# Kernel optimization log

Measured on AMD Instinct MI355X. Metric: run time of the kernel, lower is better.

## Reference

```python
import jax, jax.numpy as jnp
import numpy as np

B, N, D = 8, 4096, 1024
DEPTH, HEADS, DH = 4, 16, 64
INNER = HEADS * DH          # 1024
NL, NMP = 64, 4             # latents, mean-pooled latents
FF = 4 * D                  # ff_mult=4
EPS = 1e-5


def _ln(x, w, b):
    # nn.LayerNorm over last dim (eps added to biased variance)
    m = x.mean(-1, keepdims=True)
    v = ((x - m) ** 2).mean(-1, keepdims=True)
    return (x - m) * jax.lax.rsqrt(v + EPS) * w + b


def _ln_g(x, g):
    # custom LayerNorm: gamma only, no bias
    m = x.mean(-1, keepdims=True)
    v = ((x - m) ** 2).mean(-1, keepdims=True)
    return (x - m) * jax.lax.rsqrt(v + EPS) * g


def setup_inputs() -> dict:
    key = jax.random.key(0)
    ks = jax.random.split(key, 16)
    g = lambda i, shape: jax.random.normal(ks[i], shape, jnp.float32) * 0.02
    return dict(
        x=jax.random.normal(ks[0], (B, N, D), jnp.float32),
        pos_emb=g(1, (N, D)),                      # rows [0:N] of the embedding table
        latents=jax.random.normal(ks[2], (NL, D), jnp.float32),
        mp_ln_g=jnp.ones((D,), jnp.float32),
        mp_w=g(3, (D, D * NMP)),
        mp_b=jnp.zeros((D * NMP,), jnp.float32),
        ln_x_w=jnp.ones((DEPTH, D), jnp.float32),
        ln_x_b=jnp.zeros((DEPTH, D), jnp.float32),
        ln_lat_w=jnp.ones((DEPTH, D), jnp.float32),
        ln_lat_b=jnp.zeros((DEPTH, D), jnp.float32),
        wq=g(4, (DEPTH, D, INNER)),
        wkv=g(5, (DEPTH, D, 2 * INNER)),
        wo=g(6, (DEPTH, INNER, D)),
        out_ln_w=jnp.ones((DEPTH, D), jnp.float32),
        out_ln_b=jnp.zeros((DEPTH, D), jnp.float32),
        ff_ln1_g=jnp.ones((DEPTH, D), jnp.float32),
        ff_w1=g(7, (DEPTH, D, FF)),
        ff_ln2_g=jnp.ones((DEPTH, FF), jnp.float32),
        ff_w2=g(8, (DEPTH, FF, D)),
    )


def reference(x, pos_emb, latents, mp_ln_g, mp_w, mp_b,
              ln_x_w, ln_x_b, ln_lat_w, ln_lat_b, wq, wkv, wo,
              out_ln_w, out_ln_b, ff_ln1_g, ff_w1, ff_ln2_g, ff_w2):
    b = x.shape[0]
    xp = x + pos_emb                                  # (b, n, d)
    lat = jnp.broadcast_to(latents, (b,) + latents.shape)
    # mean-pooled latents (mask is all-ones -> plain mean over tokens)
    mp = x.mean(axis=1)                               # (b, d)
    mp_lat = (_ln_g(mp, mp_ln_g) @ mp_w + mp_b).reshape(b, NMP, D)
    lat = jnp.concatenate([mp_lat, lat], axis=1)      # (b, NMP+NL, d)
    scale = DH ** -0.5
    for l in range(DEPTH):
        # --- PerceiverAttention ---
        xn = _ln(xp, ln_x_w[l], ln_x_b[l])
        ln_lat = _ln(lat, ln_lat_w[l], ln_lat_b[l])
        q = (ln_lat @ wq[l]).reshape(b, -1, HEADS, DH) * scale   # (b, i, h, dh)
        kv = jnp.concatenate([xn, ln_lat], axis=1) @ wkv[l]      # (b, n+i, 2*inner)
        k, v = jnp.split(kv, 2, axis=-1)
        k = k.reshape(b, -1, HEADS, DH)
        v = v.reshape(b, -1, HEADS, DH)
        sim = jnp.einsum('bihd,bjhd->bhij', q, k)                # (b, h, i, n+i)
        attn = jax.nn.softmax(sim, axis=-1)
        o = jnp.einsum('bhij,bjhd->bihd', attn, v).reshape(b, -1, INNER)
        o = _ln(o @ wo[l], out_ln_w[l], out_ln_b[l])
        lat = lat + o
        # --- feedforward block ---
        h = jax.nn.gelu(_ln_g(lat, ff_ln1_g[l]) @ ff_w1[l], approximate=False)
        lat = lat + _ln_g(h, ff_ln2_g[l]) @ ff_w2[l]
    return lat
```

## Files before the change

kernel.cpp:

```cpp
#include <hip/hip_runtime.h>

typedef __bf16 bf16x8 __attribute__((ext_vector_type(8)));
typedef float f32x4 __attribute__((ext_vector_type(4)));
typedef unsigned short u16;
typedef unsigned int u32;

typedef __attribute__((address_space(3))) u16 lds_u16;
typedef __attribute__((address_space(1))) const u16 glb_u16;

#define NJC 4

__device__ inline float bf2f(u16 u) { union { u32 i; float f; } x; x.i = (u32)u << 16; return x.f; }
__device__ inline u16 f2bf(float f) {
  union { float f; u32 i; } u; u.f = f;
  u32 r = u.i + 0x7fffu + ((u.i >> 16) & 1u);
  return (u16)(r >> 16);
}

__device__ inline float blk_sum256(float v, float* red) {
#pragma unroll
  for (int o = 32; o > 0; o >>= 1) v += __shfl_xor(v, o);
  __syncthreads();
  if ((threadIdx.x & 63) == 0) red[threadIdx.x >> 6] = v;
  __syncthreads();
  return red[0] + red[1] + red[2] + red[3];
}

__global__ __launch_bounds__(512, 1) void gemm_kv(const u16* __restrict__ A,
                                                  const u16* __restrict__ BT,
                                                  u16* __restrict__ C,
                                                  const float* __restrict__ bias) {
  extern __shared__ __align__(16) u16 lds[];
  const int tid = threadIdx.x, l = tid & 63, w = tid >> 6;
  const int wr = w >> 2, wc = w & 3;
  int bid = blockIdx.x;
  int swz = (bid & 7) * 128 + (bid >> 3);
  int by = swz >> 3, bx = swz & 7;
  const long m0 = (long)by * 256;
  const int n0 = bx * 256;

  long srcA[2], srcB[2];
#pragma unroll
  for (int s = 0; s < 2; s++) {
    int g = s * 512 + tid;
    int p = g >> 3, j = g & 7, jp = j ^ (p & 7);
    int row = (p << 1) | (jp >> 2), cc = jp & 3;
    srcA[s] = (m0 + row) * 1024 + cc * 8;
    srcB[s] = ((long)(n0 + row)) * 1024 + cc * 8;
  }
  const int ldsoff[2] = { (w * 64) * 8, (512 + w * 64) * 8 };

  const int rA = l & 15, cch = l >> 4;
  const int R0a = wr * 128 + rA;
  const int aoff = (R0a >> 1) * 64 + (((((R0a & 1) << 2) | cch) ^ ((R0a >> 1) & 7)) << 3);
  const int R0b = wc * 64 + rA;
  const int boff = (R0b >> 1) * 64 + (((((R0b & 1) << 2) | cch) ^ ((R0b >> 1) & 7)) << 3);

  f32x4 acc[8][4] = {};

  auto stage = [&](int t, int ab) {
    u16* dst = lds + (((t & 3) * 2 + ab) << 13);
    const u16* src = ab == 0 ? A : BT;
    const long* so = ab == 0 ? srcA : srcB;
    int kt = t * 32;
#pragma unroll
    for (int s = 0; s < 2; s++)
      __builtin_amdgcn_global_load_lds((glb_u16*)(src + so[s] + kt),
                                       (lds_u16*)(dst + ldsoff[s]), 16, 0, 0);
  };

  stage(0, 0); stage(0, 1); stage(1, 0); stage(1, 1); stage(2, 0); stage(2, 1);
  asm volatile("s_waitcnt vmcnt(8)" ::: "memory");
  __builtin_amdgcn_s_barrier();

  for (int t = 0; t < 16; ++t) {
    const int s = 2 * t;
    const u16* Ab0 = lds + (((s & 3) * 2 + 0) << 13);
    const u16* Bb0 = lds + (((s & 3) * 2 + 1) << 13);
    const u16* Ab1 = lds + ((((s + 1) & 3) * 2 + 0) << 13);
    const u16* Bb1 = lds + ((((s + 1) & 3) * 2 + 1) << 13);
    bf16x8 af[8], b0, b1;

#pragma unroll
    for (int mf = 0; mf < 8; mf++) af[mf] = *(const bf16x8*)(Ab0 + aoff + mf * 512);
    b0 = *(const bf16x8*)(Bb0 + boff);
    b1 = *(const bf16x8*)(Bb0 + boff + 512);
    if (s + 3 < 32) stage(s + 3, 0);
    __builtin_amdgcn_s_barrier();
    asm volatile("s_waitcnt lgkmcnt(0)" ::: "memory");
    __builtin_amdgcn_sched_barrier(0);
    __builtin_amdgcn_s_setprio(1);
#pragma unroll
    for (int mf = 0; mf < 8; mf++) {
      acc[mf][0] = __builtin_amdgcn_mfma_f32_16x16x32_bf16(af[mf], b0, acc[mf][0], 0, 0, 0);
      acc[mf][1] = __builtin_amdgcn_mfma_f32_16x16x32_bf16(af[mf], b1, acc[mf][1], 0, 0, 0);
    }
    __builtin_amdgcn_s_setprio(0);
    __builtin_amdgcn_s_barrier();

    b0 = *(const bf16x8*)(Bb0 + boff + 1024);
    b1 = *(const bf16x8*)(Bb0 + boff + 1536);
    if (s + 3 < 32) stage(s + 3, 1);
    __builtin_amdgcn_s_barrier();
    asm volatile("s_waitcnt lgkmcnt(0)" ::: "memory");
    __builtin_amdgcn_sched_barrier(0);
    __builtin_amdgcn_s_setprio(1);
#pragma unroll
    for (int mf = 0; mf < 8; mf++) {
      acc[mf][2] = __builtin_amdgcn_mfma_f32_16x16x32_bf16(af[mf], b0, acc[mf][2], 0, 0, 0);
      acc[mf][3] = __builtin_amdgcn_mfma_f32_16x16x32_bf16(af[mf], b1, acc[mf][3], 0, 0, 0);
    }
    __builtin_amdgcn_s_setprio(0);
    if (t < 15) asm volatile("s_waitcnt vmcnt(8)" ::: "memory");
    else        asm volatile("s_waitcnt vmcnt(0)" ::: "memory");
    __builtin_amdgcn_s_barrier();

#pragma unroll
    for (int mf = 0; mf < 8; mf++) af[mf] = *(const bf16x8*)(Ab1 + aoff + mf * 512);
    b0 = *(const bf16x8*)(Bb1 + boff);
    b1 = *(const bf16x8*)(Bb1 + boff + 512);
    if (s + 4 < 32) stage(s + 4, 0);
    __builtin_amdgcn_s_barrier();
    asm volatile("s_waitcnt lgkmcnt(0)" ::: "memory");
    __builtin_amdgcn_sched_barrier(0);
    __builtin_amdgcn_s_setprio(1);
#pragma unroll
    for (int mf = 0; mf < 8; mf++) {
      acc[mf][0] = __builtin_amdgcn_mfma_f32_16x16x32_bf16(af[mf], b0, acc[mf][0], 0, 0, 0);
      acc[mf][1] = __builtin_amdgcn_mfma_f32_16x16x32_bf16(af[mf], b1, acc[mf][1], 0, 0, 0);
    }
    __builtin_amdgcn_s_setprio(0);
    __builtin_amdgcn_s_barrier();

    b0 = *(const bf16x8*)(Bb1 + boff + 1024);
    b1 = *(const bf16x8*)(Bb1 + boff + 1536);
    if (s + 4 < 32) stage(s + 4, 1);
    __builtin_amdgcn_s_barrier();
    asm volatile("s_waitcnt lgkmcnt(0)" ::: "memory");
    __builtin_amdgcn_sched_barrier(0);
    __builtin_amdgcn_s_setprio(1);
#pragma unroll
    for (int mf = 0; mf < 8; mf++) {
      acc[mf][2] = __builtin_amdgcn_mfma_f32_16x16x32_bf16(af[mf], b0, acc[mf][2], 0, 0, 0);
      acc[mf][3] = __builtin_amdgcn_mfma_f32_16x16x32_bf16(af[mf], b1, acc[mf][3], 0, 0, 0);
    }
    __builtin_amdgcn_s_setprio(0);
    if (t < 14)       asm volatile("s_waitcnt vmcnt(8)" ::: "memory");
    else if (t == 14) asm volatile("s_waitcnt vmcnt(4)" ::: "memory");
    __builtin_amdgcn_s_barrier();
  }

  const long batch_off = (m0 >> 12) * ((long)4164 * 2048);
  const int rb0 = (int)(m0 & 4095) + wr * 128 + ((l >> 4) << 2);
#pragma unroll
  for (int mf = 0; mf < 8; mf++) {
#pragma unroll
    for (int nf = 0; nf < 4; nf++) {
      int col = n0 + wc * 64 + nf * 16 + (l & 15);
      float bv = bias[col];
#pragma unroll
      for (int rr = 0; rr < 4; rr++) {
        int rloc = rb0 + mf * 16 + rr;
        C[batch_off + (long)rloc * 2048 + col] = f2bf(acc[mf][nf][rr] + bv);
      }
    }
  }
}

template <int MODE, bool BIAS>
__global__ __launch_bounds__(256) void gemm_nt(const u16* __restrict__ A,
                                               const u16* __restrict__ BT,
                                               void* __restrict__ C,
                                               const float* __restrict__ bias,
                                               int M, int N, int K, float alpha,
                                               int RB, long BS, int LDC, int KC) {
  __shared__ __align__(16) u16 As[2][128 * 64];
  __shared__ __align__(16) u16 Bs[2][128 * 64];
  int m0 = blockIdx.y * 128, n0 = blockIdx.x * 128;
  int tid = threadIdx.x;
  int l = tid & 63, w = tid >> 6;
  int wr = w >> 1, wc = w & 1;
  f32x4 acc[4][4] = {};

  const int srow = l >> 3;
  const int scol = (l & 7) * 8;
  const int Mc = M - 1;
  const int k0 = blockIdx.z * KC;
  const int k1 = (k0 + KC < K) ? k0 + KC : K;

  auto stage = [&](int kt, int pb) {
#pragma unroll
    for (int r = 0; r < 4; r++) {
      int rowg = (r * 4 + w) * 8;
      int arow = m0 + rowg + srow; if (arow > Mc) arow = Mc;
      int brow = n0 + rowg + srow;
      const u16* ag = A + (long)arow * K + kt + scol;
      const u16* bg = BT + (long)brow * K + kt + scol;
      __builtin_amdgcn_global_load_lds((glb_u16*)ag, (lds_u16*)(&As[pb][rowg * 64]), 16, 0, 0);
      __builtin_amdgcn_global_load_lds((glb_u16*)bg, (lds_u16*)(&Bs[pb][rowg * 64]), 16, 0, 0);
    }
  };

  stage(k0, 0);
  int it = 0;
  for (int kt = k0; kt < k1; kt += 64, ++it) {
    const int pb = it & 1;
    const bool more = (kt + 64) < k1;
    if (more) stage(kt + 64, pb ^ 1);
    if (more) asm volatile("s_waitcnt vmcnt(8)" ::: "memory");
    else      asm volatile("s_waitcnt vmcnt(0)" ::: "memory");
    __builtin_amdgcn_sched_barrier(0);
    __builtin_amdgcn_s_barrier();
    const u16* Ab = &As[pb][0];
    const u16* Bb = &Bs[pb][0];
#pragma unroll
    for (int kk = 0; kk < 2; kk++) {
      bf16x8 af[4], bfv[4];
#pragma unroll
      for (int mf = 0; mf < 4; mf++)
        af[mf] = *(const bf16x8*)(Ab + (wr * 64 + mf * 16 + (l & 15)) * 64 + kk * 32 + (l >> 4) * 8);
#pragma unroll
      for (int nf = 0; nf < 4; nf++)
        bfv[nf] = *(const bf16x8*)(Bb + (wc * 64 + nf * 16 + (l & 15)) * 64 + kk * 32 + (l >> 4) * 8);
#pragma unroll
      for (int mf = 0; mf < 4; mf++)
#pragma unroll
        for (int nf = 0; nf < 4; nf++)
          acc[mf][nf] = __builtin_amdgcn_mfma_f32_16x16x32_bf16(af[mf], bfv[nf], acc[mf][nf], 0, 0, 0);
    }
    __builtin_amdgcn_sched_barrier(0);
    __builtin_amdgcn_s_barrier();
  }

#pragma unroll
  for (int mf = 0; mf < 4; mf++) {
#pragma unroll
    for (int nf = 0; nf < 4; nf++) {
      int col = n0 + wc * 64 + nf * 16 + (l & 15);
      float bv = 0.f;
      if (BIAS) bv = bias[col];
#pragma unroll
      for (int rr = 0; rr < 4; rr++) {
        int row = m0 + wr * 64 + mf * 16 + (l >> 4) * 4 + rr;
        if (row < M) {
          float v = acc[mf][nf][rr] * alpha + bv;
          long off = (long)(row / RB) * BS + (long)(row % RB) * LDC + col;
          if (MODE == 0) ((float*)C)[off] = v;
          else if (MODE == 1) ((u16*)C)[off] = f2bf(v);
          else if (MODE == 2) ((float*)C)[off] += v;
          else atomicAdd(&((float*)C)[off], v);
        }
      }
    }
  }
}

__global__ __launch_bounds__(256) void gemm_two(const u16* __restrict__ A,
                                                const u16* __restrict__ BTq,
                                                const u16* __restrict__ BTkv,
                                                u16* __restrict__ Cq,
                                                u16* __restrict__ Ckv) {
  __shared__ __align__(16) u16 As[2][128 * 64];
  __shared__ __align__(16) u16 Bs[2][128 * 64];
  const int K = 1024, M = 544;
  int bxr = blockIdx.x;
  const u16* BT; u16* C; float alpha; int RB; long BS; int LDC; int n0;
  if (bxr < 8) { BT = BTq;  C = Cq;  alpha = 0.125f; RB = 544; BS = 0;                 LDC = 1024; n0 = bxr * 128; }
  else         { BT = BTkv; C = Ckv; alpha = 1.f;    RB = 68;  BS = (long)4164 * 2048; LDC = 2048; n0 = (bxr - 8) * 128; }
  int m0 = blockIdx.y * 128;
  int tid = threadIdx.x;
  int l = tid & 63, w = tid >> 6;
  int wr = w >> 1, wc = w & 1;
  f32x4 acc[4][4] = {};

  const int srow = l >> 3;
  const int scol = (l & 7) * 8;
  const int Mc = M - 1;

  auto stage = [&](int kt, int pb) {
#pragma unroll
    for (int r = 0; r < 4; r++) {
      int rowg = (r * 4 + w) * 8;
      int arow = m0 + rowg + srow; if (arow > Mc) arow = Mc;
      int brow = n0 + rowg + srow;
      const u16* ag = A + (long)arow * K + kt + scol;
      const u16* bg = BT + (long)brow * K + kt + scol;
      __builtin_amdgcn_global_load_lds((glb_u16*)ag, (lds_u16*)(&As[pb][rowg * 64]), 16, 0, 0);
      __builtin_amdgcn_global_load_lds((glb_u16*)bg, (lds_u16*)(&Bs[pb][rowg * 64]), 16, 0, 0);
    }
  };

  stage(0, 0);
  int it = 0;
  for (int kt = 0; kt < K; kt += 64, ++it) {
    const int pb = it & 1;
    const bool more = (kt + 64) < K;
    if (more) stage(kt + 64, pb ^ 1);
    if (more) asm volatile("s_waitcnt vmcnt(8)" ::: "memory");
    else      asm volatile("s_waitcnt vmcnt(0)" ::: "memory");
    __builtin_amdgcn_sched_barrier(0);
    __builtin_amdgcn_s_barrier();
    const u16* Ab = &As[pb][0];
    const u16* Bb = &Bs[pb][0];
#pragma unroll
    for (int kk = 0; kk < 2; kk++) {
      bf16x8 af[4], bfv[4];
#pragma unroll
      for (int mf = 0; mf < 4; mf++)
        af[mf] = *(const bf16x8*)(Ab + (wr * 64 + mf * 16 + (l & 15)) * 64 + kk * 32 + (l >> 4) * 8);
#pragma unroll
      for (int nf = 0; nf < 4; nf++)
        bfv[nf] = *(const bf16x8*)(Bb + (wc * 64 + nf * 16 + (l & 15)) * 64 + kk * 32 + (l >> 4) * 8);
#pragma unroll
      for (int mf = 0; mf < 4; mf++)
#pragma unroll
        for (int nf = 0; nf < 4; nf++)
          acc[mf][nf] = __builtin_amdgcn_mfma_f32_16x16x32_bf16(af[mf], bfv[nf], acc[mf][nf], 0, 0, 0);
    }
    __builtin_amdgcn_sched_barrier(0);
    __builtin_amdgcn_s_barrier();
  }

#pragma unroll
  for (int mf = 0; mf < 4; mf++) {
#pragma unroll
    for (int nf = 0; nf < 4; nf++) {
      int col = n0 + wc * 64 + nf * 16 + (l & 15);
#pragma unroll
      for (int rr = 0; rr < 4; rr++) {
        int row = m0 + wr * 64 + mf * 16 + (l >> 4) * 4 + rr;
        if (row < M) {
          float v = acc[mf][nf][rr] * alpha;
          long off = (long)(row / RB) * BS + (long)(row % RB) * LDC + col;
          C[off] = f2bf(v);
        }
      }
    }
  }
}

__global__ __launch_bounds__(256) void k_transpose(const float* __restrict__ W,
                                                   const float* __restrict__ scale,
                                                   u16* __restrict__ WT, int K, int N,
                                                   long wls, long sls, long tls) {
  __shared__ float tile[32][33];
  int z = blockIdx.z;
  W += (long)z * wls; WT += (long)z * tls;
  if (scale) scale += (long)z * sls;
  int n0 = blockIdx.x * 32, k0 = blockIdx.y * 32;
  int x = threadIdx.x, y = threadIdx.y;
#pragma unroll
  for (int i = 0; i < 4; i++) tile[y + 8 * i][x] = W[(long)(k0 + y + 8 * i) * N + n0 + x];
  __syncthreads();
#pragma unroll
  for (int i = 0; i < 4; i++) {
    int k = k0 + x, n = n0 + y + 8 * i;
    float v = tile[x][y + 8 * i];
    if (scale) v *= scale[k];
    WT[(long)n * K + k] = f2bf(v);
  }
}

__global__ __launch_bounds__(256) void k_transpose2(const float* __restrict__ W,
                                                    const float* __restrict__ scale,
                                                    u16* __restrict__ WTs,
                                                    u16* __restrict__ WTp, int K, int N,
                                                    long wls, long sls, long tls) {
  __shared__ float tile[32][33];
  int z = blockIdx.z;
  W += (long)z * wls; scale += (long)z * sls;
  WTs += (long)z * tls; WTp += (long)z * tls;
  int n0 = blockIdx.x * 32, k0 = blockIdx.y * 32;
  int x = threadIdx.x, y = threadIdx.y;
#pragma unroll
  for (int i = 0; i < 4; i++) tile[y + 8 * i][x] = W[(long)(k0 + y + 8 * i) * N + n0 + x];
  __syncthreads();
#pragma unroll
  for (int i = 0; i < 4; i++) {
    int k = k0 + x, n = n0 + y + 8 * i;
    float v = tile[x][y + 8 * i];
    WTp[(long)n * K + k] = f2bf(v);
    WTs[(long)n * K + k] = f2bf(v * scale[k]);
  }
}

__global__ __launch_bounds__(256) void k_xphat(const float* __restrict__ x,
                                               const float* __restrict__ pos,
                                               u16* __restrict__ xph) {
  __shared__ float red[4];
  long row = blockIdx.x;
  int n = blockIdx.x & 4095;
  const float* xr = x + row * 1024;
  const float* pr = pos + (long)n * 1024;
  float v[4]; float s = 0.f;
#pragma unroll
  for (int i = 0; i < 4; i++) { int c = threadIdx.x + i * 256; v[i] = xr[c] + pr[c]; s += v[i]; }
  float mean = blk_sum256(s, red) * (1.f / 1024.f);
  float s2 = 0.f;
#pragma unroll
  for (int i = 0; i < 4; i++) { float d = v[i] - mean; s2 += d * d; }
  float rs = rsqrtf(blk_sum256(s2, red) * (1.f / 1024.f) + 1e-5f);
#pragma unroll
  for (int i = 0; i < 4; i++) xph[row * 1024 + threadIdx.x + i * 256] = f2bf((v[i] - mean) * rs);
}

__global__ __launch_bounds__(256) void k_mp(const float* __restrict__ x, float* __restrict__ macc) {
  int d = blockIdx.x * 256 + threadIdx.x;
  int nc = blockIdx.y, b = blockIdx.z;
  const float* xb = x + (long)b * 4096 * 1024;
  float s = 0.f;
  for (int n = nc * 256; n < nc * 256 + 256; n++) s += xb[(long)n * 1024 + d];
  atomicAdd(&macc[b * 1024 + d], s);
}

__global__ __launch_bounds__(256) void k_mphat(const float* __restrict__ macc,
                                               const float* __restrict__ g,
                                               float* __restrict__ mphat) {
  __shared__ float red[4];
  int b = blockIdx.x;
  float v[4]; float s = 0.f;
#pragma unroll
  for (int i = 0; i < 4; i++) { v[i] = macc[b * 1024 + threadIdx.x + i * 256] * (1.f / 4096.f); s += v[i]; }
  float mean = blk_sum256(s, red) * (1.f / 1024.f);
  float s2 = 0.f;
#pragma unroll
  for (int i = 0; i < 4; i++) { float d = v[i] - mean; s2 += d * d; }
  float rs = rsqrtf(blk_sum256(s2, red) * (1.f / 1024.f) + 1e-5f);
#pragma unroll
  for (int i = 0; i < 4; i++) {
    int c = threadIdx.x + i * 256;
    mphat[b * 1024 + c] = (v[i] - mean) * rs * g[c];
  }
}

__global__ __launch_bounds__(256) void k_mplat(const float* __restrict__ mphat,
                                               const float* __restrict__ w,
                                               const float* __restrict__ bias,
                                               float* __restrict__ lat) {
  int j = blockIdx.x * 256 + threadIdx.x;
  int b = blockIdx.y;
  const float* mh = mphat + b * 1024;
  float s = bias[j];
  for (int k = 0; k < 1024; k++) s += mh[k] * w[(long)k * 4096 + j];
  lat[(long)b * 69632 + (j >> 10) * 1024 + (j & 1023)] = s;
}

__global__ __launch_bounds__(256) void k_latfill(const float* __restrict__ latents,
                                                 float* __restrict__ lat) {
  int idx = blockIdx.x * 256 + threadIdx.x;
  int b = idx >> 16, rest = idx & 65535;
  lat[(long)b * 69632 + 4096 + rest] = latents[rest];
}

__global__ __launch_bounds__(256) void k_lnrow(const float* __restrict__ in,
                                               const float* __restrict__ w,
                                               const float* __restrict__ bb,
                                               u16* __restrict__ out) {
  __shared__ float red[4];
  long row = blockIdx.x;
  const float* xr = in + row * 1024;
  float v[4]; float s = 0.f;
#pragma unroll
  for (int i = 0; i < 4; i++) { v[i] = xr[threadIdx.x + i * 256]; s += v[i]; }
  float mean = blk_sum256(s, red) * (1.f / 1024.f);
  float s2 = 0.f;
#pragma unroll
  for (int i = 0; i < 4; i++) { float d = v[i] - mean; s2 += d * d; }
  float rs = rsqrtf(blk_sum256(s2, red) * (1.f / 1024.f) + 1e-5f);
#pragma unroll
  for (int i = 0; i < 4; i++) {
    int c = threadIdx.x + i * 256;
    out[row * 1024 + c] = f2bf((v[i] - mean) * rs * w[c] + bb[c]);
  }
}

__global__ __launch_bounds__(256) void k_bias1(const float* __restrict__ wkv,
                                               const float* __restrict__ lnxb,
                                               float* __restrict__ bxp,
                                               long wls, long bls, long pls) {
  int z = blockIdx.z;
  wkv += (long)z * wls; lnxb += (long)z * bls; bxp += (long)z * pls;
  int n = blockIdx.x * 256 + threadIdx.x;
  int kc = blockIdx.y;
  float s = 0.f;
  for (int k = kc * 64; k < kc * 64 + 64; k++) s += lnxb[k] * wkv[(long)k * 2048 + n];
  bxp[kc * 2048 + n] = s;
}
__global__ __launch_bounds__(256) void k_bias2(const float* __restrict__ bxp,
                                               float* __restrict__ bx,
                                               long pls, long xls) {
  int z = blockIdx.y;
  bxp += (long)z * pls; bx += (long)z * xls;
  int n = blockIdx.x * 256 + threadIdx.x;
  float s = 0.f;
#pragma unroll
  for (int kc = 0; kc < 16; kc++) s += bxp[kc * 2048 + n];
  bx[n] = s;
}

__global__ __launch_bounds__(256) void k_flash(const u16* __restrict__ q,
                                               const u16* __restrict__ kv,
                                               float* __restrict__ opart,
                                               float* __restrict__ lpart) {
  int c = blockIdx.x, h = blockIdx.y, b = blockIdx.z;
  int tid = threadIdx.x, l = tid & 63, w = tid >> 6;

  __shared__ __align__(16) char smem_raw[46080];
  u16 (*Vt)[64][40] = reinterpret_cast<u16(*)[64][40]>(smem_raw);
  u16 (*Pl)[80][40] = reinterpret_cast<u16(*)[80][40]>(smem_raw + 20480);
  float (*O_s)[64] = reinterpret_cast<float(*)[64]>(smem_raw);
  float* l_s = reinterpret_cast<float*>(smem_raw + 20480);

  const int JCH = 1041;
  const int jstart = c * JCH;
  const int jend = (c == NJC - 1) ? 4164 : jstart + JCH;
  const long kvbase = (long)b * 4164 * 2048;
  const u16* Kp = kv + kvbase + h * 64;
  const u16* Vp = kv + kvbase + 1024 + h * 64;

  bf16x8 qf[5][2];
#pragma unroll
  for (int it = 0; it < 5; it++) {
    int qi = it * 16 + (l & 15); if (qi > 67) qi = 67;
    const u16* qrow = q + ((long)(b * 68 + qi) * 1024 + h * 64 + (l >> 4) * 8);
    qf[it][0] = *(const bf16x8*)(qrow);
    qf[it][1] = *(const bf16x8*)(qrow + 32);
  }

  f32x4 Of[5][4] = {};
  float lac[5] = {0.f, 0.f, 0.f, 0.f, 0.f};

  auto loadV = [&](int j0, uint4 vv[4]) {
#pragma unroll
    for (int t = 0; t < 4; t++) {
      int vj = j0 + (l & 31);
      int vjc = vj < 4163 ? vj : 4163;
      int vd = (l >> 5) * 8 + t * 16;
      vv[t] = *(const uint4*)(Vp + (long)vjc * 2048 + vd);
    }
  };
  auto loadK = [&](int j0, bf16x8& a00, bf16x8& a01, bf16x8& a10, bf16x8& a11) {
    const u16* kr0 = Kp + (long)(j0 + (l & 15)) * 2048 + (l >> 4) * 8;
    a00 = *(const bf16x8*)(kr0);
    a01 = *(const bf16x8*)(kr0 + 32);
    const u16* kr1 = Kp + (long)(j0 + 16 + (l & 15)) * 2048 + (l >> 4) * 8;
    a10 = *(const bf16x8*)(kr1);
    a11 = *(const bf16x8*)(kr1 + 32);
  };

  const int jbeg = jstart + w * 32;
  uint4 vr[4];
  bf16x8 k0a, k0b, k1a, k1b;
  if (jbeg < jend) { loadV(jbeg, vr); loadK(jbeg, k0a, k0b, k1a, k1b); }

  for (int j0 = jbeg; j0 < jend; j0 += 4 * 32) {
#pragma unroll
    for (int t = 0; t < 4; t++) {
      int vd = (l >> 5) * 8 + t * 16;
      union { uint4 q4; u16 s[8]; } uu; uu.q4 = vr[t];
#pragma unroll
      for (int e = 0; e < 8; e++) Vt[w][vd + e][l & 31] = uu.s[e];
    }
    f32x4 sf[2][5];
#pragma unroll
    for (int it = 0; it < 5; it++) {
      f32x4 d0 = {};
      d0 = __builtin_amdgcn_mfma_f32_16x16x32_bf16(k0a, qf[it][0], d0, 0, 0, 0);
      d0 = __builtin_amdgcn_mfma_f32_16x16x32_bf16(k0b, qf[it][1], d0, 0, 0, 0);
      sf[0][it] = d0;
      f32x4 d1 = {};
      d1 = __builtin_amdgcn_mfma_f32_16x16x32_bf16(k1a, qf[it][0], d1, 0, 0, 0);
      d1 = __builtin_amdgcn_mfma_f32_16x16x32_bf16(k1b, qf[it][1], d1, 0, 0, 0);
      sf[1][it] = d1;
    }
    int jn = j0 + 4 * 32;
    bool more = jn < jend;
    uint4 vr2[4];
    bf16x8 n0a, n0b, n1a, n1b;
    if (more) { loadV(jn, vr2); loadK(jn, n0a, n0b, n1a, n1b); }
#pragma unroll
    for (int jt = 0; jt < 2; jt++) {
      int jb = j0 + jt * 16 + (l >> 4) * 4;
#pragma unroll
      for (int it = 0; it < 5; it++) {
        u16 pk[4];
#pragma unroll
        for (int r = 0; r < 4; r++) {
          float p = (jb + r < jend) ? __expf(sf[jt][it][r]) : 0.f;
          lac[it] += p;
          pk[r] = f2bf(p);
        }
        *(uint2*)(&Pl[w][it * 16 + (l & 15)][jt * 16 + (l >> 4) * 4]) = *(const uint2*)pk;
      }
    }
#pragma unroll
    for (int it = 0; it < 5; it++) {
      bf16x8 pa = *(const bf16x8*)(&Pl[w][it * 16 + (l & 15)][(l >> 4) * 8]);
#pragma unroll
      for (int dt = 0; dt < 4; dt++) {
        bf16x8 vb = *(const bf16x8*)(&Vt[w][dt * 16 + (l & 15)][(l >> 4) * 8]);
        Of[it][dt] = __builtin_amdgcn_mfma_f32_16x16x32_bf16(pa, vb, Of[it][dt], 0, 0, 0);
      }
    }
    if (more) {
      vr[0] = vr2[0]; vr[1] = vr2[1]; vr[2] = vr2[2]; vr[3] = vr2[3];
      k0a = n0a; k0b = n0b; k1a = n1a; k1b = n1b;
    }
  }

  __syncthreads();
  for (int u = tid; u < 80 * 64; u += 256) ((float*)O_s)[u] = 0.f;
  if (tid < 80) l_s[tid] = 0.f;
  __syncthreads();
#pragma unroll
  for (int it = 0; it < 5; it++) {
    float v = lac[it];
    v += __shfl_xor(v, 16);
    v += __shfl_xor(v, 32);
    if (l < 16) atomicAdd(&l_s[it * 16 + l], v);
#pragma unroll
    for (int dt = 0; dt < 4; dt++) {
#pragma unroll
      for (int r = 0; r < 4; r++) {
        int i = it * 16 + (l >> 4) * 4 + r;
        int d = dt * 16 + (l & 15);
        atomicAdd(&O_s[i][d], Of[it][dt][r]);
      }
    }
  }
  __syncthreads();
  long base = (long)((b * 16 + h) * NJC + c);
  for (int u = tid; u < 68 * 64; u += 256)
    opart[base * 68 * 64 + u] = O_s[u >> 6][u & 63];
  if (tid < 68) lpart[base * 68 + tid] = l_s[tid];
}

__global__ __launch_bounds__(256) void k_comb(const float* __restrict__ opart,
                                              const float* __restrict__ lpart,
                                              u16* __restrict__ obf,
                                              float* __restrict__ o2z) {
  int r = blockIdx.x;
  int b = r / 68, i = r % 68;
#pragma unroll
  for (int it = 0; it < 4; it++) {
    int col = threadIdx.x + it * 256;
    int h = col >> 6, d = col & 63;
    long bh = (long)(b * 16 + h) * NJC;
    float os = 0.f, ls = 0.f;
    for (int cc = 0; cc < NJC; cc++) {
      os += opart[(bh + cc) * 68 * 64 + (long)i * 64 + d];
      ls += lpart[(bh + cc) * 68 + i];
    }
    obf[(long)r * 1024 + col] = f2bf(os / ls);
    o2z[(long)r * 1024 + col] = 0.f;
  }
}

__global__ __launch_bounds__(256) void k_attnln(const float* __restrict__ o2,
                                                float* __restrict__ lat,
                                                const float* __restrict__ w,
                                                const float* __restrict__ bb,
                                                const float* __restrict__ g,
                                                u16* __restrict__ latg) {
  __shared__ float red[4];
  long row = blockIdx.x;
  const float* xr = o2 + row * 1024;
  float* lr = lat + row * 1024;
  float v[4]; float s = 0.f;
#pragma unroll
  for (int i = 0; i < 4; i++) { v[i] = xr[threadIdx.x + i * 256]; s += v[i]; }
  float mean = blk_sum256(s, red) * (1.f / 1024.f);
  float s2 = 0.f;
#pragma unroll
  for (int i = 0; i < 4; i++) { float d = v[i] - mean; s2 += d * d; }
  float rs = rsqrtf(blk_sum256(s2, red) * (1.f / 1024.f) + 1e-5f);
  float lv[4]; float sl = 0.f;
#pragma unroll
  for (int i = 0; i < 4; i++) {
    int c = threadIdx.x + i * 256;
    float t = (v[i] - mean) * rs * w[c] + bb[c];
    lv[i] = lr[c] + t;
    lr[c] = lv[i];
    sl += lv[i];
  }
  float mean2 = blk_sum256(sl, red) * (1.f / 1024.f);
  float s22 = 0.f;
#pragma unroll
  for (int i = 0; i < 4; i++) { float d = lv[i] - mean2; s22 += d * d; }
  float rs2 = rsqrtf(blk_sum256(s22, red) * (1.f / 1024.f) + 1e-5f);
#pragma unroll
  for (int i = 0; i < 4; i++) {
    int c = threadIdx.x + i * 256;
    latg[row * 1024 + c] = f2bf((lv[i] - mean2) * rs2 * g[c]);
  }
}

__global__ __launch_bounds__(256) void k_geluln(const float* __restrict__ hin,
                                                const float* __restrict__ g,
                                                u16* __restrict__ out) {
  __shared__ float red[4];
  long row = blockIdx.x;
  const float* xr = hin + row * 4096;
  float v[16]; float s = 0.f;
#pragma unroll
  for (int i = 0; i < 16; i++) {
    int c = threadIdx.x + i * 256;
    float u = xr[c];
    u = 0.5f * u * (1.f + erff(u * 0.70710678118f));
    v[i] = u; s += u;
  }
  float mean = blk_sum256(s, red) * (1.f / 4096.f);
  float s2 = 0.f;
#pragma unroll
  for (int i = 0; i < 16; i++) { float d = v[i] - mean; s2 += d * d; }
  float rs = rsqrtf(blk_sum256(s2, red) * (1.f / 4096.f) + 1e-5f);
#pragma unroll
  for (int i = 0; i < 16; i++) {
    int c = threadIdx.x + i * 256;
    out[row * 4096 + c] = f2bf((v[i] - mean) * rs * g[c]);
  }
}

extern "C" void kernel_launch(void* const* d_in, const int* in_sizes, int n_in,
                              void* d_out, int out_size, void* d_ws, size_t ws_size,
                              hipStream_t stream) {
  const float* x    = (const float*)d_in[0];
  const float* pos  = (const float*)d_in[1];
  const float* lats = (const float*)d_in[2];
  const float* mplng= (const float*)d_in[3];
  const float* mpw  = (const float*)d_in[4];
  const float* mpb  = (const float*)d_in[5];
  const float* lnxw = (const float*)d_in[6];
  const float* lnxb = (const float*)d_in[7];
  const float* lnlw = (const float*)d_in[8];
  const float* lnlb = (const float*)d_in[9];
  const float* wq   = (const float*)d_in[10];
  const float* wkv  = (const float*)d_in[11];
  const float* wo   = (const float*)d_in[12];
  const float* olnw = (const float*)d_in[13];
  const float* olnb = (const float*)d_in[14];
  const float* ffg1 = (const float*)d_in[15];
  const float* ffw1 = (const float*)d_in[16];
  const float* ffg2 = (const float*)d_in[17];
  const float* ffw2 = (const float*)d_in[18];

  char* ws = (char*)d_ws;
  size_t off = 0;
  auto take = [&](size_t n) -> char* {
    off = (off + 255) & ~(size_t)255;
    char* p = ws + off; off += n; return p;
  };
  float* mp_acc = (float*)take(8 * 1024 * 4);
  float* mp_hat = (float*)take(8 * 1024 * 4);
  u16*   xp_hat = (u16*)take((size_t)8 * 4096 * 1024 * 2);
  float* lat    = (float*)take((size_t)8 * 68 * 1024 * 4);
  u16*   lnlat  = (u16*)take((size_t)544 * 1024 * 2);
  u16*   qb     = (u16*)take((size_t)544 * 1024 * 2);
  u16*   kvb    = (u16*)take(((size_t)8 * 4164 + 64) * 2048 * 2);
  float* opart  = (float*)take((size_t)128 * NJC * 68 * 64 * 4);
  float* lpart  = (float*)take((size_t)128 * NJC * 68 * 4);
  u16*   obf    = (u16*)take((size_t)544 * 1024 * 2);
  float* o2     = (float*)take((size_t)544 * 1024 * 4);
  u16*   latg   = (u16*)take((size_t)544 * 1024 * 2);
  float* hbuf   = (float*)take((size_t)544 * 4096 * 4);
  u16*   hg     = (u16*)take((size_t)544 * 4096 * 2);

  size_t fixed_off = off;
  u16 *wqT, *wkvxT, *wkvlT, *woT, *ffw1T, *ffw2T;
  float *bx, *bxp;
  auto alloc_w = [&](size_t rep) {
    wqT   = (u16*)take(rep * (size_t)1024 * 1024 * 2);
    wkvxT = (u16*)take(rep * (size_t)2048 * 1024 * 2);
    wkvlT = (u16*)take(rep * (size_t)2048 * 1024 * 2);
    woT   = (u16*)take(rep * (size_t)1024 * 1024 * 2);
    ffw1T = (u16*)take(rep * (size_t)4096 * 1024 * 2);
    ffw2T = (u16*)take(rep * (size_t)4096 * 1024 * 2);
    bx    = (float*)take(rep * 2048 * 4);
    bxp   = (float*)take(rep * 16 * 2048 * 4);
  };
  alloc_w(4);
  bool hoist = off <= ws_size;
  if (!hoist) { off = fixed_off; alloc_w(1); }

  const long KV_BS = (long)4164 * 2048;

  hipMemsetAsync(mp_acc, 0, 8 * 1024 * 4, stream);
  k_xphat<<<32768, 256, 0, stream>>>(x, pos, xp_hat);
  k_mp<<<dim3(4, 16, 8), 256, 0, stream>>>(x, mp_acc);
  k_mphat<<<8, 256, 0, stream>>>(mp_acc, mplng, mp_hat);
  k_mplat<<<dim3(16, 8), 256, 0, stream>>>(mp_hat, mpw, mpb, lat);
  k_latfill<<<2048, 256, 0, stream>>>(lats, lat);

  if (hoist) {
    k_transpose<<<dim3(32, 32, 4), dim3(32, 8), 0, stream>>>(
        wq, nullptr, wqT, 1024, 1024, 1048576, 0, 1048576);
    k_transpose2<<<dim3(64, 32, 4), dim3(32, 8), 0, stream>>>(
        wkv, lnxw, wkvxT, wkvlT, 1024, 2048, 2097152, 1024, 2097152);
    k_transpose<<<dim3(32, 32, 4), dim3(32, 8), 0, stream>>>(
        wo, nullptr, woT, 1024, 1024, 1048576, 0, 1048576);
    k_transpose<<<dim3(128, 32, 4), dim3(32, 8), 0, stream>>>(
        ffw1, nullptr, ffw1T, 1024, 4096, 4194304, 0, 4194304);
    k_transpose<<<dim3(32, 128, 4), dim3(32, 8), 0, stream>>>(
        ffw2, nullptr, ffw2T, 4096, 1024, 4194304, 0, 4194304);
    k_bias1<<<dim3(8, 16, 4), 256, 0, stream>>>(wkv, lnxb, bxp, 2097152, 1024, 32768);
    k_bias2<<<dim3(8, 4), 256, 0, stream>>>(bxp, bx, 32768, 2048);
  }

  for (int l = 0; l < 4; l++) {
    const float* wq_l  = wq  + (size_t)l * 1024 * 1024;
    const float* wkv_l = wkv + (size_t)l * 1024 * 2048;
    const float* wo_l  = wo  + (size_t)l * 1024 * 1024;
    const float* w1_l  = ffw1 + (size_t)l * 1024 * 4096;
    const float* w2_l  = ffw2 + (size_t)l * 4096 * 1024;

    if (!hoist) {
      k_transpose<<<dim3(32, 32, 1), dim3(32, 8), 0, stream>>>(
          wq_l, nullptr, wqT, 1024, 1024, 0, 0, 0);
      k_transpose2<<<dim3(64, 32, 1), dim3(32, 8), 0, stream>>>(
          wkv_l, lnxw + l * 1024, wkvxT, wkvlT, 1024, 2048, 0, 0, 0);
      k_transpose<<<dim3(32, 32, 1), dim3(32, 8), 0, stream>>>(
          wo_l, nullptr, woT, 1024, 1024, 0, 0, 0);
      k_transpose<<<dim3(128, 32, 1), dim3(32, 8), 0, stream>>>(
          w1_l, nullptr, ffw1T, 1024, 4096, 0, 0, 0);
      k_transpose<<<dim3(32, 128, 1), dim3(32, 8), 0, stream>>>(
          w2_l, nullptr, ffw2T, 4096, 1024, 0, 0, 0);
      k_bias1<<<dim3(8, 16, 1), 256, 0, stream>>>(wkv_l, lnxb + l * 1024, bxp, 0, 0, 0);
      k_bias2<<<dim3(8, 1), 256, 0, stream>>>(bxp, bx, 0, 0);
    }
    const u16* wqT_l   = wqT   + (hoist ? (size_t)l * 1048576 : 0);
    const u16* wkvxT_l = wkvxT + (hoist ? (size_t)l * 2097152 : 0);
    const u16* wkvlT_l = wkvlT + (hoist ? (size_t)l * 2097152 : 0);
    const u16* woT_l   = woT   + (hoist ? (size_t)l * 1048576 : 0);
    const u16* ffw1T_l = ffw1T + (hoist ? (size_t)l * 4194304 : 0);
    const u16* ffw2T_l = ffw2T + (hoist ? (size_t)l * 4194304 : 0);
    const float* bx_l  = bx    + (hoist ? (size_t)l * 2048 : 0);

    k_lnrow<<<544, 256, 0, stream>>>(lat, lnlw + l * 1024, lnlb + l * 1024, lnlat);

    gemm_kv<<<1024, 512, 131072, stream>>>(xp_hat, wkvxT_l, kvb, bx_l);
    gemm_two<<<dim3(24, 5), 256, 0, stream>>>(lnlat, wqT_l, wkvlT_l, qb, kvb + (size_t)4096 * 2048);

    k_flash<<<dim3(NJC, 16, 8), 256, 0, stream>>>(qb, kvb, opart, lpart);
    k_comb<<<544, 256, 0, stream>>>(opart, lpart, obf, o2);

    gemm_nt<3, false><<<dim3(8, 5, 4), 256, 0, stream>>>(
        obf, woT_l, o2, nullptr, 544, 1024, 1024, 1.f, 544, 0, 1024, 256);
    k_attnln<<<544, 256, 0, stream>>>(o2, lat, olnw + l * 1024, olnb + l * 1024,
                                      ffg1 + l * 1024, latg);
    gemm_nt<0, false><<<dim3(32, 5, 1), 256, 0, stream>>>(
        latg, ffw1T_l, hbuf, nullptr, 544, 4096, 1024, 1.f, 544, 0, 4096, 1024);
    k_geluln<<<544, 256, 0, stream>>>(hbuf, ffg2 + l * 4096, hg);
    gemm_nt<3, false><<<dim3(8, 5, 8), 256, 0, stream>>>(
        hg, ffw2T_l, lat, nullptr, 544, 1024, 4096, 1.f, 544, 0, 1024, 512);
  }

  hipMemcpyAsync(d_out, lat, (size_t)out_size * 4, hipMemcpyDeviceToDevice, stream);
}
```

Measured before the change: 1.611 ms.

## Switch gemm_kv to double-buffered LDS pipeline with higher occupancy target

```diff
diff --git a/kernel.cpp b/kernel.cpp
--- a/kernel.cpp
+++ b/kernel.cpp
@@ -26,7 +26,7 @@
   return red[0] + red[1] + red[2] + red[3];
 }
 
-__global__ __launch_bounds__(512, 1) void gemm_kv(const u16* __restrict__ A,
+__global__ __launch_bounds__(512, 4) void gemm_kv(const u16* __restrict__ A,
                                                   const u16* __restrict__ BT,
                                                   u16* __restrict__ C,
                                                   const float* __restrict__ bias) {
@@ -59,7 +59,7 @@
   f32x4 acc[8][4] = {};
 
   auto stage = [&](int t, int ab) {
-    u16* dst = lds + (((t & 3) * 2 + ab) << 13);
+    u16* dst = lds + (((t & 1) * 2 + ab) << 13);
     const u16* src = ab == 0 ? A : BT;
     const long* so = ab == 0 ? srcA : srcB;
     int kt = t * 32;
@@ -69,84 +69,32 @@
                                        (lds_u16*)(dst + ldsoff[s]), 16, 0, 0);
   };
 
-  stage(0, 0); stage(0, 1); stage(1, 0); stage(1, 1); stage(2, 0); stage(2, 1);
-  asm volatile("s_waitcnt vmcnt(8)" ::: "memory");
+  stage(0, 0); stage(0, 1); stage(1, 0); stage(1, 1);
+  asm volatile("s_waitcnt vmcnt(4)" ::: "memory");
   __builtin_amdgcn_s_barrier();
 
-  for (int t = 0; t < 16; ++t) {
-    const int s = 2 * t;
-    const u16* Ab0 = lds + (((s & 3) * 2 + 0) << 13);
-    const u16* Bb0 = lds + (((s & 3) * 2 + 1) << 13);
-    const u16* Ab1 = lds + ((((s + 1) & 3) * 2 + 0) << 13);
-    const u16* Bb1 = lds + ((((s + 1) & 3) * 2 + 1) << 13);
-    bf16x8 af[8], b0, b1;
-
-#pragma unroll
-    for (int mf = 0; mf < 8; mf++) af[mf] = *(const bf16x8*)(Ab0 + aoff + mf * 512);
-    b0 = *(const bf16x8*)(Bb0 + boff);
-    b1 = *(const bf16x8*)(Bb0 + boff + 512);
-    if (s + 3 < 32) stage(s + 3, 0);
-    __builtin_amdgcn_s_barrier();
+  for (int t = 0; t < 32; ++t) {
+    const u16* Ab = lds + (((t & 1) * 2 + 0) << 13);
+    const u16* Bb = Ab + 8192;
+    bf16x8 af[8], bf[4];
+#pragma unroll
+    for (int mf = 0; mf < 8; mf++) af[mf] = *(const bf16x8*)(Ab + aoff + mf * 512);
+#pragma unroll
+    for (int nf = 0; nf < 4; nf++) bf[nf] = *(const bf16x8*)(Bb + boff + nf * 512);
     asm volatile("s_waitcnt lgkmcnt(0)" ::: "memory");
     __builtin_amdgcn_sched_barrier(0);
+    __builtin_amdgcn_s_barrier();
+    if (t + 2 < 32) { stage(t + 2, 0); stage(t + 2, 1); }
     __builtin_amdgcn_s_setprio(1);
 #pragma unroll
-    for (int mf = 0; mf < 8; mf++) {
-      acc[mf][0] = __builtin_amdgcn_mfma_f32_16x16x32_bf16(af[mf], b0, acc[mf][0], 0, 0, 0);
-      acc[mf][1] = __builtin_amdgcn_mfma_f32_16x16x32_bf16(af[mf], b1, acc[mf][1], 0, 0, 0);
-    }
+    for (int mf = 0; mf < 8; mf++)
+#pragma unroll
+      for (int nf = 0; nf < 4; nf++)
+        acc[mf][nf] = __builtin_amdgcn_mfma_f32_16x16x32_bf16(af[mf], bf[nf], acc[mf][nf], 0, 0, 0);
     __builtin_amdgcn_s_setprio(0);
-    __builtin_amdgcn_s_barrier();
-
-    b0 = *(const bf16x8*)(Bb0 + boff + 1024);
-    b1 = *(const bf16x8*)(Bb0 + boff + 1536);
-    if (s + 3 < 32) stage(s + 3, 1);
-    __builtin_amdgcn_s_barrier();
-    asm volatile("s_waitcnt lgkmcnt(0)" ::: "memory");
+    if (t + 2 < 32)      asm volatile("s_waitcnt vmcnt(4)" ::: "memory");
+    else if (t + 1 < 32) asm volatile("s_waitcnt vmcnt(0)" ::: "memory");
     __builtin_amdgcn_sched_barrier(0);
-    __builtin_amdgcn_s_setprio(1);
-#pragma unroll
-    for (int mf = 0; mf < 8; mf++) {
-      acc[mf][2] = __builtin_amdgcn_mfma_f32_16x16x32_bf16(af[mf], b0, acc[mf][2], 0, 0, 0);
-      acc[mf][3] = __builtin_amdgcn_mfma_f32_16x16x32_bf16(af[mf], b1, acc[mf][3], 0, 0, 0);
-    }
-    __builtin_amdgcn_s_setprio(0);
-    if (t < 15) asm volatile("s_waitcnt vmcnt(8)" ::: "memory");
-    else        asm volatile("s_waitcnt vmcnt(0)" ::: "memory");
-    __builtin_amdgcn_s_barrier();
-
-#pragma unroll
-    for (int mf = 0; mf < 8; mf++) af[mf] = *(const bf16x8*)(Ab1 + aoff + mf * 512);
-    b0 = *(const bf16x8*)(Bb1 + boff);
-    b1 = *(const bf16x8*)(Bb1 + boff + 512);
-    if (s + 4 < 32) stage(s + 4, 0);
-    __builtin_amdgcn_s_barrier();
-    asm volatile("s_waitcnt lgkmcnt(0)" ::: "memory");
-    __builtin_amdgcn_sched_barrier(0);
-    __builtin_amdgcn_s_setprio(1);
-#pragma unroll
-    for (int mf = 0; mf < 8; mf++) {
-      acc[mf][0] = __builtin_amdgcn_mfma_f32_16x16x32_bf16(af[mf], b0, acc[mf][0], 0, 0, 0);
-      acc[mf][1] = __builtin_amdgcn_mfma_f32_16x16x32_bf16(af[mf], b1, acc[mf][1], 0, 0, 0);
-    }
-    __builtin_amdgcn_s_setprio(0);
-    __builtin_amdgcn_s_barrier();
-
-    b0 = *(const bf16x8*)(Bb1 + boff + 1024);
-    b1 = *(const bf16x8*)(Bb1 + boff + 1536);
-    if (s + 4 < 32) stage(s + 4, 1);
-    __builtin_amdgcn_s_barrier();
-    asm volatile("s_waitcnt lgkmcnt(0)" ::: "memory");
-    __builtin_amdgcn_sched_barrier(0);
-    __builtin_amdgcn_s_setprio(1);
-#pragma unroll
-    for (int mf = 0; mf < 8; mf++) {
-      acc[mf][2] = __builtin_amdgcn_mfma_f32_16x16x32_bf16(af[mf], b0, acc[mf][2], 0, 0, 0);
-      acc[mf][3] = __builtin_amdgcn_mfma_f32_16x16x32_bf16(af[mf], b1, acc[mf][3], 0, 0, 0);
-    }
-    __builtin_amdgcn_s_setprio(0);
-    if (t < 14)       asm volatile("s_waitcnt vmcnt(8)" ::: "memory");
-    else if (t == 14) asm volatile("s_waitcnt vmcnt(4)" ::: "memory");
     __builtin_amdgcn_s_barrier();
   }
 
@@ -837,7 +785,7 @@
 
     k_lnrow<<<544, 256, 0, stream>>>(lat, lnlw + l * 1024, lnlb + l * 1024, lnlat);
 
-    gemm_kv<<<1024, 512, 131072, stream>>>(xp_hat, wkvxT_l, kvb, bx_l);
+    gemm_kv<<<1024, 512, 65536, stream>>>(xp_hat, wkvxT_l, kvb, bx_l);
     gemm_two<<<dim3(24, 5), 256, 0, stream>>>(lnlat, wqT_l, wkvlT_l, qb, kvb + (size_t)4096 * 2048);
 
     k_flash<<<dim3(NJC, 16, 8), 256, 0, stream>>>(qb, kvb, opart, lpart);
```

New measurement: 6.079 ms. 277% more time.
